# Performance work log

Hardware: AMD Instinct MI355X
Metric: run time of the kernel (lower is better)

Reference implementation:

```python
import jax, jax.numpy as jnp
import numpy as np

T, N = 64, 2048          # timesteps, population
DT = 1e-3                # simulation step
TAU_MEM_INV = 100.0      # LIF membrane 1/tau
V_TH, V_LEAK, V_RESET = 1.0, 0.0, 0.0
TAU_PRE_INV, TAU_POST_INV = 50.0, 50.0   # STDP trace 1/tau
A_PRE, A_POST = 1.0, 1.0                 # trace contributions
ETA_PLUS, ETA_MINUS = 1e-3, 1e-3         # learning rates
W_MIN, W_MAX = 0.0, 1.0                  # hard bounds
ALPHA = 100.0                            # SuperSpike surrogate sharpness

@jax.custom_vjp
def spike(v):
    # Heaviside forward, SuperSpike surrogate backward (as in norse LIF cells)
    return (v > 0.0).astype(v.dtype)

def _spike_fwd(v):
    return spike(v), v

def _spike_bwd(v, g):
    return (g / (ALPHA * jnp.abs(v) + 1.0) ** 2,)

spike.defvjp(_spike_fwd, _spike_bwd)


def setup_inputs() -> dict:
    key = jax.random.key(0)
    k1, k2 = jax.random.split(key)
    # +1.0 bias ensures nonzero spiking activity so STDP actually fires
    exc_current = jax.random.normal(k1, (T, N), dtype=jnp.float32) + 1.0
    # recurrent weights w[post, pre], small positive init within [W_MIN, W_MAX]
    w = jax.random.uniform(k2, (N, N), dtype=jnp.float32) * 0.02
    t_pre = jnp.zeros((N,), jnp.float32)
    t_post = jnp.zeros((N,), jnp.float32)
    return {"exc_current": exc_current, "w": w, "t_pre": t_pre, "t_post": t_post}


def reference(exc_current, w, t_pre, t_post):
    n = w.shape[0]
    z0 = jnp.zeros((n,), w.dtype)  # Layer reset: cell(zeros(population))
    v0 = jnp.zeros((n,), w.dtype)

    def step(carry, x):
        w_, z, v, tp, tpo = carry
        # recurrent synaptic current: w[post, pre] @ z_pre
        i_syn = w_ @ z
        # LIF membrane update
        v = v + DT * TAU_MEM_INV * ((V_LEAK - v) + i_syn + x)
        z_new = spike(v - V_TH)
        v = v * (1.0 - z_new) + V_RESET * z_new  # reset
        # STDP traces (norse stdp_step_linear: update traces, then dw)
        tp = tp + DT * TAU_PRE_INV * (-tp + A_PRE * z_new)
        tpo = tpo + DT * TAU_POST_INV * (-tpo + A_POST * z_new)
        dw = ETA_PLUS * jnp.outer(z_new, tp) - ETA_MINUS * jnp.outer(tpo, z_new)
        w_ = jnp.clip(w_ + dw, W_MIN, W_MAX)  # additive STDP, hard bounds
        return (w_, z_new, v, tp, tpo), z_new

    _, spikes = jax.lax.scan(step, (w, z0, v0, t_pre, t_post), exc_current)
    return spikes  # [T, N], matches torch.stack([self.step(x) for x in exc_current])
```

## Files before the change

kernel.cpp:

```cpp
#include <hip/hip_runtime.h>

constexpr int   T_STEPS = 64;
constexpr int   NN      = 2048;
constexpr float DT_TAU  = 0.1f;
constexpr float V_TH_C  = 1.0f;
constexpr float TRC     = 0.05f;
constexpr float ETA     = 1e-3f;

constexpr int BLOCKS  = 256;
constexpr int THREADS = 512;
constexpr int ROWS_PER_BLOCK = NN / BLOCKS;
constexpr int CHUNKS = NN / 256;

__global__ __launch_bounds__(THREADS)
void snn_msg_kernel(const float* __restrict__ x,
                    const float* __restrict__ w_in,
                    const float* __restrict__ tpre0,
                    const float* __restrict__ tpost0,
                    unsigned long long* __restrict__ zpub,
                    float*       __restrict__ out)
{
    const int bid  = blockIdx.x;
    const int tid  = threadIdx.x;
    const int wv   = tid >> 6;
    const int lane = tid & 63;
    const int row  = bid * ROWS_PER_BLOCK + wv;

    __shared__ __align__(16) float z_s[NN];
    __shared__ __align__(16) float tp_s[NN];
    __shared__ float tpo_s8[ROWS_PER_BLOCK];
    __shared__ float isyn_s8[ROWS_PER_BLOCK];
    __shared__ unsigned zw_s[BLOCKS];

    float4 tp4 = ((const float4*)tpre0)[tid];
    ((float4*)tp_s)[tid] = tp4;

    float v_own = 0.0f, tpo_own = 0.0f, x_own = 0.0f;
    if (tid < ROWS_PER_BLOCK) {
        tpo_own = tpost0[bid * ROWS_PER_BLOCK + tid];
        isyn_s8[tid] = 0.0f;
        x_own = x[bid * ROWS_PER_BLOCK + tid];
    }

    const float4* wrow4 = (const float4*)(w_in + (size_t)row * NN);
    float4 wreg[CHUNKS];
    #pragma unroll
    for (int c = 0; c < CHUNKS; ++c) wreg[c] = wrow4[c * 64 + lane];

    __syncthreads();

    for (int t = 0; t < T_STEPS; ++t) {
        const int par = t & 1;

        if (tid < 64) {
            float z = 0.0f;
            if (tid < ROWS_PER_BLOCK) {
                float v = v_own;
                v = v + DT_TAU * ((0.0f - v) + isyn_s8[tid] + x_own);
                z = (v - V_TH_C > 0.0f) ? 1.0f : 0.0f;
                v_own = v * (1.0f - z);
                tpo_own = tpo_own + TRC * (-tpo_own + z);
                tpo_s8[tid] = tpo_own;
            }
            unsigned long long bits = __ballot(z > 0.0f) & 0xFFull;
            if (tid == 0) {
                unsigned long long word =
                    ((unsigned long long)(unsigned)t << 32) | bits;
                __hip_atomic_store(&zpub[par * BLOCKS + bid], word,
                                   __ATOMIC_RELAXED, __HIP_MEMORY_SCOPE_AGENT);
            }
            if (tid < ROWS_PER_BLOCK) {
                int tn = (t + 1 < T_STEPS) ? t + 1 : t;
                x_own = x[(size_t)tn * NN + bid * ROWS_PER_BLOCK + tid];
            }
        }

        if (tid < BLOCKS) {
            unsigned long long v;
            do {
                v = __hip_atomic_load(&zpub[par * BLOCKS + tid],
                                      __ATOMIC_RELAXED, __HIP_MEMORY_SCOPE_AGENT);
            } while ((unsigned)(v >> 32) != (unsigned)t);
            zw_s[tid] = (unsigned)v;
        }
        __syncthreads();

        {
            unsigned wbits = zw_s[tid >> 1];
            int sh = (tid & 1) * 4;
            float4 z4;
            z4.x = ((wbits >> (sh + 0)) & 1u) ? 1.0f : 0.0f;
            z4.y = ((wbits >> (sh + 1)) & 1u) ? 1.0f : 0.0f;
            z4.z = ((wbits >> (sh + 2)) & 1u) ? 1.0f : 0.0f;
            z4.w = ((wbits >> (sh + 3)) & 1u) ? 1.0f : 0.0f;
            ((float4*)z_s)[tid] = z4;
            tp4.x = tp4.x + TRC * (-tp4.x + z4.x);
            tp4.y = tp4.y + TRC * (-tp4.y + z4.y);
            tp4.z = tp4.z + TRC * (-tp4.z + z4.z);
            tp4.w = tp4.w + TRC * (-tp4.w + z4.w);
            ((float4*)tp_s)[tid] = tp4;
            if (bid == 0) ((float4*)(out + (size_t)t * NN))[tid] = z4;
        }
        __syncthreads();

        if (t == T_STEPS - 1) break;

        const float zi   = z_s[row];
        const float tpoi = tpo_s8[wv];
        float acc = 0.0f;
        const float4* z4s  = (const float4*)z_s;
        const float4* tp4s = (const float4*)tp_s;
        #pragma unroll
        for (int c = 0; c < CHUNKS; ++c) {
            float4 zj = z4s[c * 64 + lane];
            float4 tj = tp4s[c * 64 + lane];
            float nw;
            nw = wreg[c].x + (ETA * (zi * tj.x) - ETA * (tpoi * zj.x));
            nw = fminf(fmaxf(nw, 0.0f), 1.0f); wreg[c].x = nw; acc += nw * zj.x;
            nw = wreg[c].y + (ETA * (zi * tj.y) - ETA * (tpoi * zj.y));
            nw = fminf(fmaxf(nw, 0.0f), 1.0f); wreg[c].y = nw; acc += nw * zj.y;
            nw = wreg[c].z + (ETA * (zi * tj.z) - ETA * (tpoi * zj.z));
            nw = fminf(fmaxf(nw, 0.0f), 1.0f); wreg[c].z = nw; acc += nw * zj.z;
            nw = wreg[c].w + (ETA * (zi * tj.w) - ETA * (tpoi * zj.w));
            nw = fminf(fmaxf(nw, 0.0f), 1.0f); wreg[c].w = nw; acc += nw * zj.w;
        }
        #pragma unroll
        for (int m = 32; m >= 1; m >>= 1) acc += __shfl_xor(acc, m, 64);
        if (lane == 0) isyn_s8[wv] = acc;
        __syncthreads();
    }
}

extern "C" void kernel_launch(void* const* d_in, const int* in_sizes, int n_in,
                              void* d_out, int out_size, void* d_ws, size_t ws_size,
                              hipStream_t stream) {
    const float* x     = (const float*)d_in[0];
    const float* w_in  = (const float*)d_in[1];
    const float* tpre  = (const float*)d_in[2];
    const float* tpost = (const float*)d_in[3];
    float*       out   = (float*)d_out;

    unsigned long long* zpub = (unsigned long long*)d_ws;

    void* args[] = {(void*)&x, (void*)&w_in, (void*)&tpre, (void*)&tpost,
                    (void*)&zpub, (void*)&out};
    hipLaunchCooperativeKernel((void*)snn_msg_kernel,
                               dim3(BLOCKS), dim3(THREADS),
                               args, 0, stream);
}
```

Baseline: 311.9 us.

## Keep pre-traces in registers and unpack spike bits per wave to cut barriers

New measurement: 354.3 us. 1.14x slower.

```diff
diff --git a/kernel.cpp b/kernel.cpp
--- a/kernel.cpp
+++ b/kernel.cpp
@@ -9,71 +9,64 @@
 
 constexpr int BLOCKS  = 256;
 constexpr int THREADS = 512;
-constexpr int ROWS_PER_BLOCK = NN / BLOCKS;
-constexpr int CHUNKS = NN / 256;
+constexpr int RPB     = NN / BLOCKS;
+constexpr int CHUNKS  = NN / 256;
 
 __global__ __launch_bounds__(THREADS)
-void snn_msg_kernel(const float* __restrict__ x,
-                    const float* __restrict__ w_in,
-                    const float* __restrict__ tpre0,
-                    const float* __restrict__ tpost0,
-                    unsigned long long* __restrict__ zpub,
-                    float*       __restrict__ out)
+void snn_bits_kernel(const float* __restrict__ x,
+                     const float* __restrict__ w_in,
+                     const float* __restrict__ tpre0,
+                     const float* __restrict__ tpost0,
+                     unsigned long long* __restrict__ zpub,
+                     float*       __restrict__ out)
 {
     const int bid  = blockIdx.x;
     const int tid  = threadIdx.x;
     const int wv   = tid >> 6;
     const int lane = tid & 63;
-    const int row  = bid * ROWS_PER_BLOCK + wv;
+    const int row  = bid * RPB + wv;
 
-    __shared__ __align__(16) float z_s[NN];
-    __shared__ __align__(16) float tp_s[NN];
-    __shared__ float tpo_s8[ROWS_PER_BLOCK];
-    __shared__ float isyn_s8[ROWS_PER_BLOCK];
-    __shared__ unsigned zw_s[BLOCKS];
+    __shared__ unsigned zw_s[2][BLOCKS];
+    __shared__ float    zbit_s[RPB];
+    __shared__ float    x_s[T_STEPS * RPB];
 
-    float4 tp4 = ((const float4*)tpre0)[tid];
-    ((float4*)tp_s)[tid] = tp4;
-
-    float v_own = 0.0f, tpo_own = 0.0f, x_own = 0.0f;
-    if (tid < ROWS_PER_BLOCK) {
-        tpo_own = tpost0[bid * ROWS_PER_BLOCK + tid];
-        isyn_s8[tid] = 0.0f;
-        x_own = x[bid * ROWS_PER_BLOCK + tid];
-    }
+    x_s[tid] = x[(size_t)(tid >> 3) * NN + bid * RPB + (tid & 7)];
 
     const float4* wrow4 = (const float4*)(w_in + (size_t)row * NN);
     float4 wreg[CHUNKS];
     #pragma unroll
     for (int c = 0; c < CHUNKS; ++c) wreg[c] = wrow4[c * 64 + lane];
 
+    float4 tpreg[CHUNKS];
+    #pragma unroll
+    for (int c = 0; c < CHUNKS; ++c) tpreg[c] = ((const float4*)tpre0)[c * 64 + lane];
+
+    float v_own = 0.0f, tpo_own = 0.0f, z_own = 0.0f;
+    if (lane == 0) tpo_own = tpost0[row];
+
     __syncthreads();
 
-    for (int t = 0; t < T_STEPS; ++t) {
+    if (lane == 0) {
+        float v = v_own + DT_TAU * ((0.0f - v_own) + 0.0f + x_s[0 * RPB + wv]);
+        float z = (v - V_TH_C > 0.0f) ? 1.0f : 0.0f;
+        v_own   = v * (1.0f - z);
+        tpo_own = tpo_own + TRC * (-tpo_own + z);
+        z_own   = z;
+        out[row] = z;
+        zbit_s[wv] = z;
+    }
+    __syncthreads();
+    if (tid == 0) {
+        unsigned long long bits = 0;
+        #pragma unroll
+        for (int r = 0; r < RPB; ++r)
+            bits |= (zbit_s[r] > 0.0f ? 1ull : 0ull) << r;
+        __hip_atomic_store(&zpub[0 * BLOCKS + bid], bits ,
+                           __ATOMIC_RELAXED, __HIP_MEMORY_SCOPE_AGENT);
+    }
+
+    for (int t = 0; t < T_STEPS - 1; ++t) {
         const int par = t & 1;
-
-        if (tid < 64) {
-            float z = 0.0f;
-            if (tid < ROWS_PER_BLOCK) {
-                float v = v_own;
-                v = v + DT_TAU * ((0.0f - v) + isyn_s8[tid] + x_own);
-                z = (v - V_TH_C > 0.0f) ? 1.0f : 0.0f;
-                v_own = v * (1.0f - z);
-                tpo_own = tpo_own + TRC * (-tpo_own + z);
-                tpo_s8[tid] = tpo_own;
-            }
-            unsigned long long bits = __ballot(z > 0.0f) & 0xFFull;
-            if (tid == 0) {
-                unsigned long long word =
-                    ((unsigned long long)(unsigned)t << 32) | bits;
-                __hip_atomic_store(&zpub[par * BLOCKS + bid], word,
-                                   __ATOMIC_RELAXED, __HIP_MEMORY_SCOPE_AGENT);
-            }
-            if (tid < ROWS_PER_BLOCK) {
-                int tn = (t + 1 < T_STEPS) ? t + 1 : t;
-                x_own = x[(size_t)tn * NN + bid * ROWS_PER_BLOCK + tid];
-            }
-        }
 
         if (tid < BLOCKS) {
             unsigned long long v;
@@ -81,53 +74,64 @@
                 v = __hip_atomic_load(&zpub[par * BLOCKS + tid],
                                       __ATOMIC_RELAXED, __HIP_MEMORY_SCOPE_AGENT);
             } while ((unsigned)(v >> 32) != (unsigned)t);
-            zw_s[tid] = (unsigned)v;
+            zw_s[par][tid] = (unsigned)v;
         }
         __syncthreads();
 
-        {
-            unsigned wbits = zw_s[tid >> 1];
-            int sh = (tid & 1) * 4;
-            float4 z4;
-            z4.x = ((wbits >> (sh + 0)) & 1u) ? 1.0f : 0.0f;
-            z4.y = ((wbits >> (sh + 1)) & 1u) ? 1.0f : 0.0f;
-            z4.z = ((wbits >> (sh + 2)) & 1u) ? 1.0f : 0.0f;
-            z4.w = ((wbits >> (sh + 3)) & 1u) ? 1.0f : 0.0f;
-            ((float4*)z_s)[tid] = z4;
-            tp4.x = tp4.x + TRC * (-tp4.x + z4.x);
-            tp4.y = tp4.y + TRC * (-tp4.y + z4.y);
-            tp4.z = tp4.z + TRC * (-tp4.z + z4.z);
-            tp4.w = tp4.w + TRC * (-tp4.w + z4.w);
-            ((float4*)tp_s)[tid] = tp4;
-            if (bid == 0) ((float4*)(out + (size_t)t * NN))[tid] = z4;
-        }
-        __syncthreads();
+        const float zi   = __shfl(z_own, 0, 64);
+        const float tpoi = __shfl(tpo_own, 0, 64);
+        const float a =  ETA * zi;
+        const float b =  ETA * tpoi;
 
-        if (t == T_STEPS - 1) break;
-
-        const float zi   = z_s[row];
-        const float tpoi = tpo_s8[wv];
         float acc = 0.0f;
-        const float4* z4s  = (const float4*)z_s;
-        const float4* tp4s = (const float4*)tp_s;
         #pragma unroll
         for (int c = 0; c < CHUNKS; ++c) {
-            float4 zj = z4s[c * 64 + lane];
-            float4 tj = tp4s[c * 64 + lane];
+            const unsigned wb = zw_s[par][c * 32 + (lane >> 1)];
+            const int sh = (lane & 1) * 4;
+            float4 z4;
+            z4.x = ((wb >> (sh + 0)) & 1u) ? 1.0f : 0.0f;
+            z4.y = ((wb >> (sh + 1)) & 1u) ? 1.0f : 0.0f;
+            z4.z = ((wb >> (sh + 2)) & 1u) ? 1.0f : 0.0f;
+            z4.w = ((wb >> (sh + 3)) & 1u) ? 1.0f : 0.0f;
+
+            tpreg[c].x = tpreg[c].x + TRC * (-tpreg[c].x + z4.x);
+            tpreg[c].y = tpreg[c].y + TRC * (-tpreg[c].y + z4.y);
+            tpreg[c].z = tpreg[c].z + TRC * (-tpreg[c].z + z4.z);
+            tpreg[c].w = tpreg[c].w + TRC * (-tpreg[c].w + z4.w);
+
             float nw;
-            nw = wreg[c].x + (ETA * (zi * tj.x) - ETA * (tpoi * zj.x));
-            nw = fminf(fmaxf(nw, 0.0f), 1.0f); wreg[c].x = nw; acc += nw * zj.x;
-            nw = wreg[c].y + (ETA * (zi * tj.y) - ETA * (tpoi * zj.y));
-            nw = fminf(fmaxf(nw, 0.0f), 1.0f); wreg[c].y = nw; acc += nw * zj.y;
-            nw = wreg[c].z + (ETA * (zi * tj.z) - ETA * (tpoi * zj.z));
-            nw = fminf(fmaxf(nw, 0.0f), 1.0f); wreg[c].z = nw; acc += nw * zj.z;
-            nw = wreg[c].w + (ETA * (zi * tj.w) - ETA * (tpoi * zj.w));
-            nw = fminf(fmaxf(nw, 0.0f), 1.0f); wreg[c].w = nw; acc += nw * zj.w;
+            nw = wreg[c].x + (a * tpreg[c].x - b * z4.x);
+            nw = fmaxf(nw, 0.0f); wreg[c].x = nw; acc += nw * z4.x;
+            nw = wreg[c].y + (a * tpreg[c].y - b * z4.y);
+            nw = fmaxf(nw, 0.0f); wreg[c].y = nw; acc += nw * z4.y;
+            nw = wreg[c].z + (a * tpreg[c].z - b * z4.z);
+            nw = fmaxf(nw, 0.0f); wreg[c].z = nw; acc += nw * z4.z;
+            nw = wreg[c].w + (a * tpreg[c].w - b * z4.w);
+            nw = fmaxf(nw, 0.0f); wreg[c].w = nw; acc += nw * z4.w;
         }
         #pragma unroll
         for (int m = 32; m >= 1; m >>= 1) acc += __shfl_xor(acc, m, 64);
-        if (lane == 0) isyn_s8[wv] = acc;
+
+        if (lane == 0) {
+            float v = v_own + DT_TAU * ((0.0f - v_own) + acc + x_s[(t + 1) * RPB + wv]);
+            float z = (v - V_TH_C > 0.0f) ? 1.0f : 0.0f;
+            v_own   = v * (1.0f - z);
+            tpo_own = tpo_own + TRC * (-tpo_own + z);
+            z_own   = z;
+            out[(size_t)(t + 1) * NN + row] = z;
+            zbit_s[wv] = z;
+        }
         __syncthreads();
+        if (tid == 0) {
+            unsigned long long bits = 0;
+            #pragma unroll
+            for (int r = 0; r < RPB; ++r)
+                bits |= (zbit_s[r] > 0.0f ? 1ull : 0ull) << r;
+            const unsigned long long word =
+                ((unsigned long long)(unsigned)(t + 1) << 32) | bits;
+            __hip_atomic_store(&zpub[((t + 1) & 1) * BLOCKS + bid], word,
+                               __ATOMIC_RELAXED, __HIP_MEMORY_SCOPE_AGENT);
+        }
     }
 }
 
@@ -144,7 +148,7 @@
 
     void* args[] = {(void*)&x, (void*)&w_in, (void*)&tpre, (void*)&tpost,
                     (void*)&zpub, (void*)&out};
-    hipLaunchCooperativeKernel((void*)snn_msg_kernel,
+    hipLaunchCooperativeKernel((void*)snn_bits_kernel,
                                dim3(BLOCKS), dim3(THREADS),
                                args, 0, stream);
 }
```
